# Optimization experiments

Measured on AMD Instinct MI355X. Metric: run time of the kernel, lower is better.

## Reference

```python
import jax, jax.numpy as jnp
import numpy as np

B, S, H, DH, DM = 1024, 32, 32, 32, 1024  # seq==heads==head_dim==32 forced by module's reshapes


def setup_inputs() -> dict:
    key = jax.random.key(0)
    k1, k2 = jax.random.split(key)
    x = jax.random.normal(k1, (B, S, DM), dtype=jnp.float32)
    mask = jnp.ones((1, 1, S, DH), dtype=bool)
    W_qkv = jax.random.normal(k2, (DM, 3 * H * DH), dtype=jnp.float32) / np.sqrt(DM).astype(np.float32)
    return {"x": x, "mask": mask, "W_qkv": W_qkv}


def _rope(t, sin, cos):
    # t: [B, S, H, DH]; sin/cos: [S] broadcast over the HEADS axis (axis 2), as in the original
    t1, t2 = jnp.split(t, 2, axis=-1)
    rot = jnp.concatenate([-t2, t1], axis=-1)
    return t * cos.reshape(1, 1, -1, 1) + rot * sin.reshape(1, 1, -1, 1)


def reference(x, mask, W_qkv):
    b, seq_len, _ = x.shape
    qkv = x @ W_qkv  # [B, S, 3*H*DH]
    q, k, v = jnp.split(qkv, 3, axis=-1)
    q = q.reshape(b, -1, H, DH)
    k = k.reshape(b, -1, H, DH)
    v = v.reshape(b, -1, H, DH)
    pos = jnp.arange(seq_len, dtype=x.dtype)
    sin, cos = jnp.sin(pos), jnp.cos(pos)
    q = _rope(q, sin, cos)
    k = _rope(k, sin, cos)
    # matmul over heads axis (faithful to original): [B,S,H,DH] @ [B,S,DH,H] -> [B,S,H,H]
    attn = jnp.matmul(q, k.transpose(0, 1, 3, 2)) / jnp.sqrt(jnp.asarray(DH, x.dtype))
    attn = attn.reshape(b, H, seq_len, DH)  # valid only because H == 32
    attn = jnp.where(jnp.broadcast_to(mask, attn.shape), attn, -jnp.inf)
    attn = jax.nn.softmax(attn, axis=-1)
    out = jnp.matmul(attn, v)  # [B,H,S,DH] @ [B,S,H,DH]; batched since S==H==32
    return out.reshape(-1, seq_len, H * DH)
```

## Files before the change

### kernel.cpp

```cpp
#include <hip/hip_runtime.h>

typedef __bf16 bf16_t;
typedef __bf16 bf16x4 __attribute__((ext_vector_type(4)));
typedef __bf16 bf16x8 __attribute__((ext_vector_type(8)));
typedef float f32x4 __attribute__((ext_vector_type(4)));
typedef float f32x16 __attribute__((ext_vector_type(16)));
typedef unsigned int uint4v __attribute__((ext_vector_type(4)));

#define M_TOT 32768
#define N_TOT 3072
#define K_TOT 1024

#define WT_BYTES (3072u * 1024u * 2u)
#define XB_BYTES ((size_t)M_TOT * 1024 * 2)

__device__ __forceinline__ void gload_lds16(const void* g, void* l) {
  __builtin_amdgcn_global_load_lds(
      (const __attribute__((address_space(1))) unsigned int*)g,
      (__attribute__((address_space(3))) unsigned int*)l, 16, 0, 0);
}

__device__ __forceinline__ unsigned pk2(float a, float b) {
  unsigned short lo = __builtin_bit_cast(unsigned short, (bf16_t)a);
  unsigned short hi = __builtin_bit_cast(unsigned short, (bf16_t)b);
  return ((unsigned)hi << 16) | (unsigned)lo;
}

__global__ __launch_bounds__(256) void k_wt(const float* __restrict__ W,
                                            bf16_t* __restrict__ wt) {
  __shared__ float tile[64][65];
  const int c0 = blockIdx.x * 64, k0 = blockIdx.y * 64;
  const int t = threadIdx.x;
  for (int rep = 0; rep < 16; ++rep) {
    int lin = rep * 256 + t;
    int kl = lin >> 6, cl = lin & 63;
    tile[kl][cl] = W[(size_t)(k0 + kl) * 3072 + (c0 + cl)];
  }
  __syncthreads();
  const float scale = 0.17677669529663687f;
  for (int rep = 0; rep < 16; ++rep) {
    int lin = rep * 256 + t;
    int cl = lin >> 6, kl = lin & 63;
    int c = c0 + cl;
    float val;
    if (c < 2048) {
      int cc = c & 1023;
      int h = cc >> 5, d = cc & 31;
      float cv = cosf((float)h), sv = sinf((float)h);
      int clp = cl + ((d < 16) ? 16 : -16);
      float other = tile[kl][clp];
      val = tile[kl][cl] * cv + ((d < 16) ? -other : other) * sv;
      if (c < 1024) val *= scale;
    } else {
      val = tile[kl][cl];
    }
    wt[(size_t)c * 1024 + (k0 + kl)] = (bf16_t)val;
  }
}

__global__ __launch_bounds__(256) void k_xb(const float* __restrict__ x,
                                            bf16_t* __restrict__ xb) {
  const size_t nf4 = (size_t)M_TOT * K_TOT / 4;
  const float4* src = (const float4*)x;
  for (size_t i = (size_t)blockIdx.x * 256 + threadIdx.x; i < nf4;
       i += (size_t)gridDim.x * 256) {
    float4 a = src[i];
    bf16x4 o;
    o[0] = (bf16_t)a.x; o[1] = (bf16_t)a.y; o[2] = (bf16_t)a.z; o[3] = (bf16_t)a.w;
    *(bf16x4*)(&xb[i * 4]) = o;
  }
}

__global__ __launch_bounds__(256) void k_gemm(const bf16_t* __restrict__ xb,
                                              const bf16_t* __restrict__ wt,
                                              bf16_t* __restrict__ qk,
                                              bf16_t* __restrict__ vb) {
  __shared__ __attribute__((aligned(16))) bf16_t Al[128 * 32];
  __shared__ __attribute__((aligned(16))) bf16_t Bl[128 * 32];
  const int t = threadIdx.x;
  const int w = t >> 6, lane = t & 63;
  const int wr = w >> 1, wc = w & 1;
  const int row0 = blockIdx.y * 128, col0 = blockIdx.x * 128;

  f32x4 acc[4][4];
  for (int m = 0; m < 4; ++m)
    for (int n = 0; n < 4; ++n)
      for (int i = 0; i < 4; ++i) acc[m][n][i] = 0.f;

  const char* abase = (const char*)xb + (size_t)row0 * 2048;
  const char* bbase = (const char*)wt + (size_t)col0 * 2048;
  const int rsel = lane & 15, ksel = (lane >> 4) * 8;

  for (int kt = 0; kt < 32; ++kt) {
    const int kbyte = kt * 64;
#pragma unroll
    for (int p = 0; p < 2; ++p) {
      const int chunk = w * 2 + p;
      const int o = chunk * 1024 + lane * 16;
      const int trow = o >> 6, twithin = o & 63;
      gload_lds16(abase + (size_t)trow * 2048 + kbyte + twithin, (char*)Al + chunk * 1024);
      gload_lds16(bbase + (size_t)trow * 2048 + kbyte + twithin, (char*)Bl + chunk * 1024);
    }
    __syncthreads();
    bf16x8 a[4], b[4];
#pragma unroll
    for (int m = 0; m < 4; ++m)
      a[m] = *(const bf16x8*)&Al[(wr * 64 + m * 16 + rsel) * 32 + ksel];
#pragma unroll
    for (int n = 0; n < 4; ++n)
      b[n] = *(const bf16x8*)&Bl[(wc * 64 + n * 16 + rsel) * 32 + ksel];
#pragma unroll
    for (int m = 0; m < 4; ++m)
#pragma unroll
      for (int n = 0; n < 4; ++n)
        acc[m][n] = __builtin_amdgcn_mfma_f32_16x16x32_bf16(a[m], b[n], acc[m][n], 0, 0, 0);
    __syncthreads();
  }

  const bool isv = (col0 >= 2048);
  const int rgrp = (lane >> 4) * 4;
#pragma unroll
  for (int m = 0; m < 4; ++m)
#pragma unroll
    for (int n = 0; n < 4; ++n)
#pragma unroll
      for (int reg = 0; reg < 4; ++reg) {
        const int R = row0 + wr * 64 + m * 16 + rgrp + reg;
        const int C = col0 + wc * 64 + n * 16 + rsel;
        const bf16_t val = (bf16_t)acc[m][n][reg];
        if (!isv) qk[(size_t)R * 2048 + C] = val;
        else      vb[(size_t)R * 1024 + (C - 2048)] = val;
      }
}

__global__ __launch_bounds__(256) void k_attn(const bf16_t* __restrict__ qk,
                                              const bf16_t* __restrict__ vb,
                                              float* __restrict__ out) {
  __shared__ __attribute__((aligned(16))) bf16_t vl[4][1024];
  const int t = threadIdx.x;
  const int w = t >> 6, lane = t & 63;
  const int r = blockIdx.x * 4 + w;
  const int jm = lane & 31, hi = lane >> 5;

  const char* vsrc = (const char*)vb + (size_t)r * 2048;
  gload_lds16(vsrc + lane * 16, (char*)vl[w]);
  gload_lds16(vsrc + 1024 + lane * 16, (char*)vl[w] + 1024);

  const char* rowbase = (const char*)qk + (size_t)r * 4096;
  const bf16x8 ak0 = *(const bf16x8*)(rowbase + 2048 + jm * 64 + hi * 16);
  const bf16x8 ak1 = *(const bf16x8*)(rowbase + 2048 + jm * 64 + 32 + hi * 16);
  const bf16x8 bq0 = *(const bf16x8*)(rowbase + jm * 64 + hi * 16);
  const bf16x8 bq1 = *(const bf16x8*)(rowbase + jm * 64 + 32 + hi * 16);

  f32x16 s;
  for (int i = 0; i < 16; ++i) s[i] = 0.f;
  s = __builtin_amdgcn_mfma_f32_32x32x16_bf16(ak0, bq0, s, 0, 0, 0);
  s = __builtin_amdgcn_mfma_f32_32x32x16_bf16(ak1, bq1, s, 0, 0, 0);

  float mx = s[0];
#pragma unroll
  for (int i = 1; i < 16; ++i) mx = fmaxf(mx, s[i]);
  mx = fmaxf(mx, __shfl_xor(mx, 32));
  float p[16];
  float sum = 0.f;
#pragma unroll
  for (int i = 0; i < 16; ++i) { p[i] = __expf(s[i] - mx); sum += p[i]; }
  sum += __shfl_xor(sum, 32);
  const float inv = 1.f / sum;
#pragma unroll
  for (int i = 0; i < 16; ++i) p[i] *= inv;

  const unsigned t01 = pk2(p[0], p[1]),  t23 = pk2(p[2], p[3]);
  const unsigned t45 = pk2(p[4], p[5]),  t67 = pk2(p[6], p[7]);
  const unsigned t89 = pk2(p[8], p[9]),  tab = pk2(p[10], p[11]);
  const unsigned tcd = pk2(p[12], p[13]), tef = pk2(p[14], p[15]);
  const unsigned x01 = (unsigned)__shfl_xor((int)t01, 32), x23 = (unsigned)__shfl_xor((int)t23, 32);
  const unsigned x45 = (unsigned)__shfl_xor((int)t45, 32), x67 = (unsigned)__shfl_xor((int)t67, 32);
  const unsigned x89 = (unsigned)__shfl_xor((int)t89, 32), xab = (unsigned)__shfl_xor((int)tab, 32);
  const unsigned xcd = (unsigned)__shfl_xor((int)tcd, 32), xef = (unsigned)__shfl_xor((int)tef, 32);
  uint4v u0, u1;
  u0[0] = hi ? x45 : t01; u0[1] = hi ? x67 : t23; u0[2] = hi ? t45 : x01; u0[3] = hi ? t67 : x23;
  u1[0] = hi ? xcd : t89; u1[1] = hi ? xef : tab; u1[2] = hi ? tcd : x89; u1[3] = hi ? tef : xab;
  const bf16x8 pa0 = __builtin_bit_cast(bf16x8, u0);
  const bf16x8 pa1 = __builtin_bit_cast(bf16x8, u1);

  asm volatile("s_waitcnt vmcnt(0)" ::: "memory");
  union { bf16x8 v; bf16_t e[8]; } v0, v1;
#pragma unroll
  for (int e = 0; e < 8; ++e) v0.e[e] = vl[w][(8 * hi + e) * 32 + jm];
#pragma unroll
  for (int e = 0; e < 8; ++e) v1.e[e] = vl[w][(16 + 8 * hi + e) * 32 + jm];

  f32x16 o;
  for (int i = 0; i < 16; ++i) o[i] = 0.f;
  o = __builtin_amdgcn_mfma_f32_32x32x16_bf16(pa0, v0.v, o, 0, 0, 0);
  o = __builtin_amdgcn_mfma_f32_32x32x16_bf16(pa1, v1.v, o, 0, 0, 0);

  float* orow = out + (size_t)r * 1024;
#pragma unroll
  for (int reg = 0; reg < 16; ++reg) {
    const int jrow = (reg & 3) + 8 * (reg >> 2) + 4 * hi;
    orow[jrow * 32 + jm] = o[reg];
  }
}

extern "C" void kernel_launch(void* const* d_in, const int* in_sizes, int n_in,
                              void* d_out, int out_size, void* d_ws, size_t ws_size,
                              hipStream_t stream) {
  const float* x = (const float*)d_in[0];
  const float* W = (const float*)d_in[2];

  char* ws = (char*)d_ws;
  bf16_t* wt = (bf16_t*)ws;
  bf16_t* xb = (bf16_t*)(ws + WT_BYTES);
  bf16_t* vb = (bf16_t*)(ws + WT_BYTES + XB_BYTES);

  k_wt <<<dim3(48, 16), 256, 0, stream>>>(W, wt);
  k_xb <<<16384, 256, 0, stream>>>(x, xb);
  k_gemm<<<dim3(24, 256), 256, 0, stream>>>(xb, wt, (bf16_t*)d_out, vb);
  k_attn<<<8192, 256, 0, stream>>>((const bf16_t*)d_out, vb, (float*)d_out);
}
```

Baseline: 338.1 us.

## Rewrite QKV GEMM with triple-buffered LDS pipeline, larger tiles, swizzled layout

Replaces the simple single-buffered GEMM with a 256x128 tile per 512-thread block and a K-step of 64 elements. Tiles flow through a three-slot LDS ring filled by direct global-to-LDS loads, with fine-grained waitcnt/barrier interleaving and raised MFMA priority. It also adds an XOR-swizzled LDS layout against bank conflicts and a block-index swizzle for L2 locality. The aim is to overlap memory loads with MFMA work and cut per-iteration sync overhead, at the cost of much more complex hand-scheduled code and fragile vmcnt accounting.

```diff
diff --git a/kernel.cpp b/kernel.cpp
--- a/kernel.cpp
+++ b/kernel.cpp
@@ -13,6 +13,11 @@
 
 #define WT_BYTES (3072u * 1024u * 2u)
 #define XB_BYTES ((size_t)M_TOT * 1024 * 2)
+
+#define BKB 128
+#define ABYTES 32768
+#define BBYTES 16384
+#define SLOT_BYTES (ABYTES + BBYTES)
 
 __device__ __forceinline__ void gload_lds16(const void* g, void* l) {
   __builtin_amdgcn_global_load_lds(
@@ -71,51 +76,136 @@
   }
 }
 
-__global__ __launch_bounds__(256) void k_gemm(const bf16_t* __restrict__ xb,
-                                              const bf16_t* __restrict__ wt,
-                                              bf16_t* __restrict__ qk,
-                                              bf16_t* __restrict__ vb) {
-  __shared__ __attribute__((aligned(16))) bf16_t Al[128 * 32];
-  __shared__ __attribute__((aligned(16))) bf16_t Bl[128 * 32];
-  const int t = threadIdx.x;
-  const int w = t >> 6, lane = t & 63;
+template <int STAGE, int BW>
+__device__ __forceinline__ void gemm_tile(char* slotR, char* slotW, int tstage,
+                                          const char* const (&asrc)[4],
+                                          const char* const (&bsrc)[2],
+                                          int w, int abase_off, int bbase_off,
+                                          int koff0, f32x4 (&acc)[4][4]) {
+  bf16x8 bfr[4][2];
+  bf16x8 af0[2][2], af1[2][2];
+  const int koff1 = koff0 ^ 64;
+
+  if constexpr (STAGE) {
+    gload_lds16(asrc[0] + (size_t)tstage * BKB, slotW + 0 * 8192 + w * 1024);
+    gload_lds16(asrc[1] + (size_t)tstage * BKB, slotW + 1 * 8192 + w * 1024);
+    gload_lds16(asrc[2] + (size_t)tstage * BKB, slotW + 2 * 8192 + w * 1024);
+  }
+#pragma unroll
+  for (int n = 0; n < 4; ++n) {
+    bfr[n][0] = *(const bf16x8*)(slotR + bbase_off + n * 2048 + koff0);
+    bfr[n][1] = *(const bf16x8*)(slotR + bbase_off + n * 2048 + koff1);
+  }
+#pragma unroll
+  for (int m = 0; m < 2; ++m) {
+    af0[m][0] = *(const bf16x8*)(slotR + abase_off + m * 2048 + koff0);
+    af0[m][1] = *(const bf16x8*)(slotR + abase_off + m * 2048 + koff1);
+  }
+  asm volatile("s_waitcnt lgkmcnt(8)" ::: "memory");
+  __builtin_amdgcn_s_barrier();
+  asm volatile("s_waitcnt lgkmcnt(0)" ::: "memory");
+  __builtin_amdgcn_sched_barrier(0);
+  __builtin_amdgcn_s_setprio(1);
+#pragma unroll
+  for (int m = 0; m < 2; ++m)
+#pragma unroll
+    for (int n = 0; n < 4; ++n) {
+      acc[m][n] = __builtin_amdgcn_mfma_f32_16x16x32_bf16(af0[m][0], bfr[n][0], acc[m][n], 0, 0, 0);
+      acc[m][n] = __builtin_amdgcn_mfma_f32_16x16x32_bf16(af0[m][1], bfr[n][1], acc[m][n], 0, 0, 0);
+    }
+  __builtin_amdgcn_s_setprio(0);
+  __builtin_amdgcn_s_barrier();
+
+  if constexpr (STAGE) {
+    gload_lds16(asrc[3] + (size_t)tstage * BKB, slotW + 3 * 8192 + w * 1024);
+    gload_lds16(bsrc[0] + (size_t)tstage * BKB, slotW + ABYTES + 0 * 8192 + w * 1024);
+    gload_lds16(bsrc[1] + (size_t)tstage * BKB, slotW + ABYTES + 1 * 8192 + w * 1024);
+  }
+#pragma unroll
+  for (int m = 0; m < 2; ++m) {
+    af1[m][0] = *(const bf16x8*)(slotR + abase_off + (m + 2) * 2048 + koff0);
+    af1[m][1] = *(const bf16x8*)(slotR + abase_off + (m + 2) * 2048 + koff1);
+  }
+  __builtin_amdgcn_s_barrier();
+  asm volatile("s_waitcnt lgkmcnt(0)" ::: "memory");
+  __builtin_amdgcn_sched_barrier(0);
+  __builtin_amdgcn_s_setprio(1);
+#pragma unroll
+  for (int m = 0; m < 2; ++m)
+#pragma unroll
+    for (int n = 0; n < 4; ++n) {
+      acc[m + 2][n] = __builtin_amdgcn_mfma_f32_16x16x32_bf16(af1[m][0], bfr[n][0], acc[m + 2][n], 0, 0, 0);
+      acc[m + 2][n] = __builtin_amdgcn_mfma_f32_16x16x32_bf16(af1[m][1], bfr[n][1], acc[m + 2][n], 0, 0, 0);
+    }
+  __builtin_amdgcn_s_setprio(0);
+  if constexpr (BW == 6) asm volatile("s_waitcnt vmcnt(6)" ::: "memory");
+  else if constexpr (BW == 0) asm volatile("s_waitcnt vmcnt(0)" ::: "memory");
+  __builtin_amdgcn_s_barrier();
+}
+
+__global__ __launch_bounds__(512, 2) void k_gemm(const bf16_t* __restrict__ xb,
+                                                 const bf16_t* __restrict__ wt,
+                                                 bf16_t* __restrict__ qk,
+                                                 bf16_t* __restrict__ vb) {
+  __shared__ __attribute__((aligned(16))) char lds[3 * SLOT_BYTES];
+  const int tid = threadIdx.x;
+  const int w = tid >> 6, lane = tid & 63;
   const int wr = w >> 1, wc = w & 1;
-  const int row0 = blockIdx.y * 128, col0 = blockIdx.x * 128;
+
+  const int bid = blockIdx.x;
+  const int swz = (bid & 7) * 384 + (bid >> 3);
+  const int tm = swz / 24, tn = swz % 24;
+  const int row0 = tm * 256, col0 = tn * 128;
+
+  const int l8 = lane >> 3, l7 = lane & 7;
+  const int awithin = (l7 * 16) ^ (l8 << 4);
+  const char* asrc[4];
+  const char* bsrc[2];
+#pragma unroll
+  for (int i = 0; i < 4; ++i)
+    asrc[i] = (const char*)xb + (size_t)(row0 + i * 64 + w * 8 + l8) * 2048 + awithin;
+#pragma unroll
+  for (int i = 0; i < 2; ++i)
+    bsrc[i] = (const char*)wt + (size_t)(col0 + i * 64 + w * 8 + l8) * 2048 + awithin;
+
+  const int rsel = lane & 15;
+  const int koff0 = ((lane >> 4) * 16) ^ (l7 << 4);
+  const int abase_off = (wr * 64 + rsel) * 128;
+  const int bbase_off = ABYTES + (wc * 64 + rsel) * 128;
 
   f32x4 acc[4][4];
+#pragma unroll
   for (int m = 0; m < 4; ++m)
+#pragma unroll
     for (int n = 0; n < 4; ++n)
+#pragma unroll
       for (int i = 0; i < 4; ++i) acc[m][n][i] = 0.f;
 
-  const char* abase = (const char*)xb + (size_t)row0 * 2048;
-  const char* bbase = (const char*)wt + (size_t)col0 * 2048;
-  const int rsel = lane & 15, ksel = (lane >> 4) * 8;
-
-  for (int kt = 0; kt < 32; ++kt) {
-    const int kbyte = kt * 64;
-#pragma unroll
-    for (int p = 0; p < 2; ++p) {
-      const int chunk = w * 2 + p;
-      const int o = chunk * 1024 + lane * 16;
-      const int trow = o >> 6, twithin = o & 63;
-      gload_lds16(abase + (size_t)trow * 2048 + kbyte + twithin, (char*)Al + chunk * 1024);
-      gload_lds16(bbase + (size_t)trow * 2048 + kbyte + twithin, (char*)Bl + chunk * 1024);
-    }
-    __syncthreads();
-    bf16x8 a[4], b[4];
-#pragma unroll
-    for (int m = 0; m < 4; ++m)
-      a[m] = *(const bf16x8*)&Al[(wr * 64 + m * 16 + rsel) * 32 + ksel];
-#pragma unroll
-    for (int n = 0; n < 4; ++n)
-      b[n] = *(const bf16x8*)&Bl[(wc * 64 + n * 16 + rsel) * 32 + ksel];
-#pragma unroll
-    for (int m = 0; m < 4; ++m)
-#pragma unroll
-      for (int n = 0; n < 4; ++n)
-        acc[m][n] = __builtin_amdgcn_mfma_f32_16x16x32_bf16(a[m], b[n], acc[m][n], 0, 0, 0);
-    __syncthreads();
-  }
+  {
+    char* s0 = lds;
+    char* s1 = lds + SLOT_BYTES;
+#pragma unroll
+    for (int i = 0; i < 4; ++i) gload_lds16(asrc[i], s0 + i * 8192 + w * 1024);
+#pragma unroll
+    for (int i = 0; i < 2; ++i) gload_lds16(bsrc[i], s0 + ABYTES + i * 8192 + w * 1024);
+#pragma unroll
+    for (int i = 0; i < 4; ++i) gload_lds16(asrc[i] + BKB, s1 + i * 8192 + w * 1024);
+#pragma unroll
+    for (int i = 0; i < 2; ++i) gload_lds16(bsrc[i] + BKB, s1 + ABYTES + i * 8192 + w * 1024);
+    asm volatile("s_waitcnt vmcnt(6)" ::: "memory");
+    __builtin_amdgcn_s_barrier();
+  }
+
+  int sr = 0;
+  for (int t = 0; t < 14; ++t) {
+    char* slotR = lds + sr * SLOT_BYTES;
+    const int swi = (sr >= 1) ? sr - 1 : 2;
+    char* slotW = lds + swi * SLOT_BYTES;
+    gemm_tile<1, 6>(slotR, slotW, t + 2, asrc, bsrc, w, abase_off, bbase_off, koff0, acc);
+    sr = (sr == 2) ? 0 : sr + 1;
+  }
+  gemm_tile<0, 0>(lds + 2 * SLOT_BYTES, lds, 0, asrc, bsrc, w, abase_off, bbase_off, koff0, acc);
+  gemm_tile<0, -1>(lds, lds, 0, asrc, bsrc, w, abase_off, bbase_off, koff0, acc);
 
   const bool isv = (col0 >= 2048);
   const int rgrp = (lane >> 4) * 4;
@@ -217,6 +307,6 @@
 
   k_wt <<<dim3(48, 16), 256, 0, stream>>>(W, wt);
   k_xb <<<16384, 256, 0, stream>>>(x, xb);
-  k_gemm<<<dim3(24, 256), 256, 0, stream>>>(xb, wt, (bf16_t*)d_out, vb);
+  k_gemm<<<3072, 512, 0, stream>>>(xb, wt, (bf16_t*)d_out, vb);
   k_attn<<<8192, 256, 0, stream>>>((const bf16_t*)d_out, vb, (float*)d_out);
 }
```

New measurement: 334.7 us. No clear change (-1.0%).

## Rewrite QKV GEMM with 256x256 tiles, double-buffered LDS and swizzled pipeline

Applied to the files above, without the earlier changes.

The QKV projection GEMM moves from 128x128 tiles with a synchronous single-buffer loop to 256x256 tiles on 512 threads, with a 64-wide K step. LDS is double-buffered, and global-to-LDS loads for the next tile are interleaved with MFMA phases under fine-grained barriers and s_setprio. It also adds an XOR swizzle on LDS addresses to avoid bank conflicts and a block-index swizzle for L2 locality. The aim is to hide memory latency and raise MFMA utilisation. In exchange, register pressure rises (128 accumulator floats per thread) and the hand-placed waitcnt/barrier ordering becomes fragile.

```diff
diff --git a/kernel.cpp b/kernel.cpp
--- a/kernel.cpp
+++ b/kernel.cpp
@@ -13,6 +13,9 @@
 
 #define WT_BYTES (3072u * 1024u * 2u)
 #define XB_BYTES ((size_t)M_TOT * 1024 * 2)
+
+#define BREG 32768
+#define SLOT 65536
 
 __device__ __forceinline__ void gload_lds16(const void* g, void* l) {
   __builtin_amdgcn_global_load_lds(
@@ -71,62 +74,178 @@
   }
 }
 
-__global__ __launch_bounds__(256) void k_gemm(const bf16_t* __restrict__ xb,
-                                              const bf16_t* __restrict__ wt,
-                                              bf16_t* __restrict__ qk,
-                                              bf16_t* __restrict__ vb) {
-  __shared__ __attribute__((aligned(16))) bf16_t Al[128 * 32];
-  __shared__ __attribute__((aligned(16))) bf16_t Bl[128 * 32];
-  const int t = threadIdx.x;
-  const int w = t >> 6, lane = t & 63;
-  const int wr = w >> 1, wc = w & 1;
-  const int row0 = blockIdx.y * 128, col0 = blockIdx.x * 128;
-
-  f32x4 acc[4][4];
+template <int FINAL>
+__device__ __forceinline__ void ktile(const char* sR, char* sW,
+                                      const char* aT, const char* bT, int w,
+                                      int aoff0, int boff0,
+                                      f32x4 (&acc)[8][4]) {
+  bf16x8 a[4][2], b[4][2];
+
+  if constexpr (!FINAL) {
+    gload_lds16(aT, sW + w * 1024);
+    gload_lds16(aT + 64 * 2048, sW + 8192 + w * 1024);
+  }
+#pragma unroll
+  for (int m = 0; m < 4; ++m) {
+    const int o = aoff0 + m * 4096;
+    a[m][0] = *(const bf16x8*)(sR + o);
+    a[m][1] = *(const bf16x8*)(sR + (o ^ 64));
+  }
+#pragma unroll
+  for (int n = 0; n < 2; ++n) {
+    const int o = boff0 + n * 8192;
+    b[n][0] = *(const bf16x8*)(sR + o);
+    b[n][1] = *(const bf16x8*)(sR + (o ^ 64));
+  }
+  asm volatile("s_waitcnt lgkmcnt(8)" ::: "memory");
+  __builtin_amdgcn_s_barrier();
+  asm volatile("s_waitcnt lgkmcnt(0)" ::: "memory");
+  __builtin_amdgcn_sched_barrier(0);
+  __builtin_amdgcn_s_setprio(1);
+#pragma unroll
   for (int m = 0; m < 4; ++m)
+#pragma unroll
+    for (int n = 0; n < 2; ++n) {
+      acc[m][n] = __builtin_amdgcn_mfma_f32_16x16x32_bf16(a[m][0], b[n][0], acc[m][n], 0, 0, 0);
+      acc[m][n] = __builtin_amdgcn_mfma_f32_16x16x32_bf16(a[m][1], b[n][1], acc[m][n], 0, 0, 0);
+    }
+  __builtin_amdgcn_s_setprio(0);
+  if constexpr (!FINAL) asm volatile("s_waitcnt vmcnt(4)" ::: "memory");
+  else                  asm volatile("s_waitcnt vmcnt(2)" ::: "memory");
+  __builtin_amdgcn_s_barrier();
+
+  if constexpr (!FINAL) {
+    gload_lds16(bT, sW + BREG + w * 1024);
+    gload_lds16(bT + 64 * 2048, sW + BREG + 8192 + w * 1024);
+  }
+#pragma unroll
+  for (int n = 2; n < 4; ++n) {
+    const int o = boff0 + n * 8192;
+    b[n][0] = *(const bf16x8*)(sR + o);
+    b[n][1] = *(const bf16x8*)(sR + (o ^ 64));
+  }
+  __builtin_amdgcn_s_barrier();
+  asm volatile("s_waitcnt lgkmcnt(0)" ::: "memory");
+  __builtin_amdgcn_sched_barrier(0);
+  __builtin_amdgcn_s_setprio(1);
+#pragma unroll
+  for (int m = 0; m < 4; ++m)
+#pragma unroll
+    for (int n = 2; n < 4; ++n) {
+      acc[m][n] = __builtin_amdgcn_mfma_f32_16x16x32_bf16(a[m][0], b[n][0], acc[m][n], 0, 0, 0);
+      acc[m][n] = __builtin_amdgcn_mfma_f32_16x16x32_bf16(a[m][1], b[n][1], acc[m][n], 0, 0, 0);
+    }
+  __builtin_amdgcn_s_setprio(0);
+  if constexpr (!FINAL) asm volatile("s_waitcnt vmcnt(4)" ::: "memory");
+  else                  asm volatile("s_waitcnt vmcnt(0)" ::: "memory");
+  __builtin_amdgcn_s_barrier();
+
+  if constexpr (!FINAL) {
+    gload_lds16(bT + 128 * 2048, sW + BREG + 16384 + w * 1024);
+    gload_lds16(bT + 192 * 2048, sW + BREG + 24576 + w * 1024);
+  }
+#pragma unroll
+  for (int m = 0; m < 4; ++m) {
+    const int o = aoff0 + (m + 4) * 4096;
+    a[m][0] = *(const bf16x8*)(sR + o);
+    a[m][1] = *(const bf16x8*)(sR + (o ^ 64));
+  }
+  __builtin_amdgcn_s_barrier();
+  asm volatile("s_waitcnt lgkmcnt(0)" ::: "memory");
+  __builtin_amdgcn_sched_barrier(0);
+  __builtin_amdgcn_s_setprio(1);
+#pragma unroll
+  for (int m = 0; m < 4; ++m)
+#pragma unroll
+    for (int n = 2; n < 4; ++n) {
+      acc[m + 4][n] = __builtin_amdgcn_mfma_f32_16x16x32_bf16(a[m][0], b[n][0], acc[m + 4][n], 0, 0, 0);
+      acc[m + 4][n] = __builtin_amdgcn_mfma_f32_16x16x32_bf16(a[m][1], b[n][1], acc[m + 4][n], 0, 0, 0);
+    }
+  __builtin_amdgcn_s_setprio(0);
+  __builtin_amdgcn_s_barrier();
+
+  if constexpr (!FINAL) {
+    gload_lds16(aT + 128 * 2048, sW + 16384 + w * 1024);
+    gload_lds16(aT + 192 * 2048, sW + 24576 + w * 1024);
+  }
+  __builtin_amdgcn_s_barrier();
+  __builtin_amdgcn_s_setprio(1);
+#pragma unroll
+  for (int m = 0; m < 4; ++m)
+#pragma unroll
+    for (int n = 0; n < 2; ++n) {
+      acc[m + 4][n] = __builtin_amdgcn_mfma_f32_16x16x32_bf16(a[m][0], b[n][0], acc[m + 4][n], 0, 0, 0);
+      acc[m + 4][n] = __builtin_amdgcn_mfma_f32_16x16x32_bf16(a[m][1], b[n][1], acc[m + 4][n], 0, 0, 0);
+    }
+  __builtin_amdgcn_s_setprio(0);
+  if constexpr (!FINAL) asm volatile("s_waitcnt vmcnt(4)" ::: "memory");
+  __builtin_amdgcn_s_barrier();
+}
+
+__global__ __launch_bounds__(512, 2) void k_gemm(const bf16_t* __restrict__ xb,
+                                                 const bf16_t* __restrict__ wt,
+                                                 bf16_t* __restrict__ qk,
+                                                 bf16_t* __restrict__ vb) {
+  __shared__ __attribute__((aligned(16))) char lds[2 * SLOT];
+  const int tid = threadIdx.x;
+  const int w = tid >> 6, lane = tid & 63;
+  const int wr = w >> 2, wc = w & 3;
+
+  const int bid = blockIdx.x;
+  const int swz = (bid & 7) * 192 + (bid >> 3);
+  const int tm = swz / 12, tn = swz % 12;
+  const int row0 = tm * 256, col0 = tn * 256;
+
+  const int l8 = lane >> 3, l7 = lane & 7;
+  const int awithin = (l7 * 16) ^ (l8 << 4);
+  const char* aT0 = (const char*)xb + (size_t)(row0 + w * 8 + l8) * 2048 + awithin;
+  const char* bT0 = (const char*)wt + (size_t)(col0 + w * 8 + l8) * 2048 + awithin;
+
+  const int rsel = lane & 15;
+  const int koff0 = ((lane >> 4) * 16) ^ (l7 << 4);
+  const int aoff0 = (wr * 16 + rsel) * 128 + koff0;
+  const int boff0 = BREG + (wc * 16 + rsel) * 128 + koff0;
+
+  f32x4 acc[8][4];
+#pragma unroll
+  for (int m = 0; m < 8; ++m)
+#pragma unroll
     for (int n = 0; n < 4; ++n)
+#pragma unroll
       for (int i = 0; i < 4; ++i) acc[m][n][i] = 0.f;
 
-  const char* abase = (const char*)xb + (size_t)row0 * 2048;
-  const char* bbase = (const char*)wt + (size_t)col0 * 2048;
-  const int rsel = lane & 15, ksel = (lane >> 4) * 8;
-
-  for (int kt = 0; kt < 32; ++kt) {
-    const int kbyte = kt * 64;
-#pragma unroll
-    for (int p = 0; p < 2; ++p) {
-      const int chunk = w * 2 + p;
-      const int o = chunk * 1024 + lane * 16;
-      const int trow = o >> 6, twithin = o & 63;
-      gload_lds16(abase + (size_t)trow * 2048 + kbyte + twithin, (char*)Al + chunk * 1024);
-      gload_lds16(bbase + (size_t)trow * 2048 + kbyte + twithin, (char*)Bl + chunk * 1024);
-    }
-    __syncthreads();
-    bf16x8 a[4], b[4];
-#pragma unroll
-    for (int m = 0; m < 4; ++m)
-      a[m] = *(const bf16x8*)&Al[(wr * 64 + m * 16 + rsel) * 32 + ksel];
-#pragma unroll
-    for (int n = 0; n < 4; ++n)
-      b[n] = *(const bf16x8*)&Bl[(wc * 64 + n * 16 + rsel) * 32 + ksel];
-#pragma unroll
-    for (int m = 0; m < 4; ++m)
-#pragma unroll
-      for (int n = 0; n < 4; ++n)
-        acc[m][n] = __builtin_amdgcn_mfma_f32_16x16x32_bf16(a[m], b[n], acc[m][n], 0, 0, 0);
-    __syncthreads();
-  }
+  {
+    char* s0 = lds;
+    gload_lds16(aT0, s0 + w * 1024);
+    gload_lds16(aT0 + 64 * 2048, s0 + 8192 + w * 1024);
+    gload_lds16(bT0, s0 + BREG + w * 1024);
+    gload_lds16(bT0 + 64 * 2048, s0 + BREG + 8192 + w * 1024);
+    gload_lds16(bT0 + 128 * 2048, s0 + BREG + 16384 + w * 1024);
+    gload_lds16(bT0 + 192 * 2048, s0 + BREG + 24576 + w * 1024);
+    gload_lds16(aT0 + 128 * 2048, s0 + 16384 + w * 1024);
+    gload_lds16(aT0 + 192 * 2048, s0 + 24576 + w * 1024);
+    asm volatile("s_waitcnt vmcnt(4)" ::: "memory");
+    __builtin_amdgcn_s_barrier();
+  }
+
+  for (int t = 0; t < 15; ++t) {
+    const char* sR = lds + (t & 1) * SLOT;
+    char* sW = lds + ((t + 1) & 1) * SLOT;
+    ktile<0>(sR, sW, aT0 + (size_t)(t + 1) * 128, bT0 + (size_t)(t + 1) * 128,
+             w, aoff0, boff0, acc);
+  }
+  ktile<1>(lds + SLOT, lds, aT0, bT0, w, aoff0, boff0, acc);
 
   const bool isv = (col0 >= 2048);
   const int rgrp = (lane >> 4) * 4;
 #pragma unroll
-  for (int m = 0; m < 4; ++m)
+  for (int m = 0; m < 8; ++m)
 #pragma unroll
     for (int n = 0; n < 4; ++n)
 #pragma unroll
       for (int reg = 0; reg < 4; ++reg) {
-        const int R = row0 + wr * 64 + m * 16 + rgrp + reg;
-        const int C = col0 + wc * 64 + n * 16 + rsel;
+        const int R = row0 + wr * 16 + m * 32 + rgrp + reg;
+        const int C = col0 + wc * 16 + n * 64 + rsel;
         const bf16_t val = (bf16_t)acc[m][n][reg];
         if (!isv) qk[(size_t)R * 2048 + C] = val;
         else      vb[(size_t)R * 1024 + (C - 2048)] = val;
@@ -217,6 +336,6 @@
 
   k_wt <<<dim3(48, 16), 256, 0, stream>>>(W, wt);
   k_xb <<<16384, 256, 0, stream>>>(x, xb);
-  k_gemm<<<dim3(24, 256), 256, 0, stream>>>(xb, wt, (bf16_t*)d_out, vb);
+  k_gemm<<<1536, 512, 0, stream>>>(xb, wt, (bf16_t*)d_out, vb);
   k_attn<<<8192, 256, 0, stream>>>((const bf16_t*)d_out, vb, (float*)d_out);
 }
```

New measurement: 292.6 us. 13.4% less time.

## Rewrite QKV GEMM with 256x256 tiles, triple-buffered LDS pipeline and swizzling

Applied to the files above, without the earlier changes.

Replaces the 128x128 single-buffered GEMM with a 512-thread 256x256-tile kernel. It uses a three-slot LDS ring fed by global_load_lds, an XOR-swizzled LDS layout, interleaved MFMA and LDS reads with setprio and sched barriers, and a block-index swizzle for L2 locality. The goal is to hide global-load latency, cut the per-iteration barrier count and raise data reuse per tile. It adds heavy register pressure from 32 accumulator tiles and fragile hand-written waitcnt sequencing.

```diff
diff --git a/kernel.cpp b/kernel.cpp
--- a/kernel.cpp
+++ b/kernel.cpp
@@ -13,6 +13,8 @@
 
 #define WT_BYTES (3072u * 1024u * 2u)
 #define XB_BYTES ((size_t)M_TOT * 1024 * 2)
+
+#define SLOT 32768
 
 __device__ __forceinline__ void gload_lds16(const void* g, void* l) {
   __builtin_amdgcn_global_load_lds(
@@ -71,62 +73,153 @@
   }
 }
 
-__global__ __launch_bounds__(256) void k_gemm(const bf16_t* __restrict__ xb,
-                                              const bf16_t* __restrict__ wt,
-                                              bf16_t* __restrict__ qk,
-                                              bf16_t* __restrict__ vb) {
-  __shared__ __attribute__((aligned(16))) bf16_t Al[128 * 32];
-  __shared__ __attribute__((aligned(16))) bf16_t Bl[128 * 32];
-  const int t = threadIdx.x;
-  const int w = t >> 6, lane = t & 63;
-  const int wr = w >> 1, wc = w & 1;
-  const int row0 = blockIdx.y * 128, col0 = blockIdx.x * 128;
-
-  f32x4 acc[4][4];
-  for (int m = 0; m < 4; ++m)
+template <int MODE>
+__device__ __forceinline__ void ktile(const char* sR, const char* sRn, char* sW,
+                                      const char* aT, const char* bT, int w,
+                                      int aoffLo, int boffLo,
+                                      f32x4 (&acc)[8][4],
+                                      bf16x8 (&a)[4], bf16x8 (&b)[4]) {
+  bf16x8 a2[4];
+
+  if constexpr (MODE == 0) gload_lds16(aT, sW + w * 1024);
+  b[2] = *(const bf16x8*)(sR + (boffLo ^ 64));
+  b[3] = *(const bf16x8*)(sR + ((boffLo + 8192) ^ 64));
+  asm volatile("s_waitcnt lgkmcnt(2)" ::: "memory");
+  __builtin_amdgcn_sched_barrier(0);
+  __builtin_amdgcn_s_setprio(1);
+#pragma unroll
+  for (int m = 0; m < 4; ++m)
+#pragma unroll
+    for (int n = 0; n < 2; ++n)
+      acc[m][n] = __builtin_amdgcn_mfma_f32_16x16x32_bf16(a[m], b[n], acc[m][n], 0, 0, 0);
+  __builtin_amdgcn_s_setprio(0);
+
+  if constexpr (MODE == 0) gload_lds16(bT, sW + 16384 + w * 1024);
+#pragma unroll
+  for (int m = 0; m < 4; ++m)
+    a2[m] = *(const bf16x8*)(sR + ((aoffLo + m * 4096) ^ 64));
+  asm volatile("s_waitcnt lgkmcnt(4)" ::: "memory");
+  __builtin_amdgcn_sched_barrier(0);
+  __builtin_amdgcn_s_setprio(1);
+#pragma unroll
+  for (int m = 0; m < 4; ++m)
+#pragma unroll
+    for (int n = 2; n < 4; ++n)
+      acc[m][n] = __builtin_amdgcn_mfma_f32_16x16x32_bf16(a[m], b[n], acc[m][n], 0, 0, 0);
+  __builtin_amdgcn_s_setprio(0);
+
+  if constexpr (MODE == 0) gload_lds16(aT + 64 * 2048, sW + 8192 + w * 1024);
+  asm volatile("s_waitcnt lgkmcnt(0)" ::: "memory");
+  __builtin_amdgcn_sched_barrier(0);
+  __builtin_amdgcn_s_setprio(1);
+#pragma unroll
+  for (int m = 0; m < 4; ++m)
+#pragma unroll
+    for (int n = 2; n < 4; ++n)
+      acc[m + 4][n] = __builtin_amdgcn_mfma_f32_16x16x32_bf16(a2[m], b[n], acc[m + 4][n], 0, 0, 0);
+  __builtin_amdgcn_s_setprio(0);
+
+  if constexpr (MODE == 0) {
+    gload_lds16(bT + 64 * 2048, sW + 24576 + w * 1024);
+    asm volatile("s_waitcnt vmcnt(4)" ::: "memory");
+  } else if constexpr (MODE == 1) {
+    asm volatile("s_waitcnt vmcnt(0)" ::: "memory");
+  }
+  if constexpr (MODE <= 1) {
+    __builtin_amdgcn_s_barrier();
+    __builtin_amdgcn_sched_barrier(0);
+#pragma unroll
+    for (int m = 0; m < 4; ++m)
+      a[m] = *(const bf16x8*)(sRn + aoffLo + m * 4096);
+    __builtin_amdgcn_sched_barrier(0);
+  }
+  __builtin_amdgcn_s_setprio(1);
+#pragma unroll
+  for (int m = 0; m < 4; ++m)
+#pragma unroll
+    for (int n = 0; n < 2; ++n)
+      acc[m + 4][n] = __builtin_amdgcn_mfma_f32_16x16x32_bf16(a2[m], b[n], acc[m + 4][n], 0, 0, 0);
+  __builtin_amdgcn_s_setprio(0);
+  if constexpr (MODE <= 1) {
+    b[0] = *(const bf16x8*)(sRn + boffLo);
+    b[1] = *(const bf16x8*)(sRn + boffLo + 8192);
+  }
+}
+
+__global__ __launch_bounds__(512, 2) void k_gemm(const bf16_t* __restrict__ xb,
+                                                 const bf16_t* __restrict__ wt,
+                                                 bf16_t* __restrict__ qk,
+                                                 bf16_t* __restrict__ vb) {
+  __shared__ __attribute__((aligned(16))) char lds[3 * SLOT];
+  const int tid = threadIdx.x;
+  const int w = tid >> 6, lane = tid & 63;
+  const int wr = w >> 2, wc = w & 3;
+
+  const int bid = blockIdx.x;
+  const int swz = (bid & 7) * 192 + (bid >> 3);
+  const int tm = swz / 12, tn = swz % 12;
+  const int row0 = tm * 256, col0 = tn * 256;
+
+  const int j = lane >> 3;
+  const int u = (lane & 7) ^ j;
+  const int half = u >> 2, kk = u & 3;
+  const char* aS = (const char*)xb + (size_t)(row0 + half * 128 + w * 8 + j) * 2048 + kk * 16;
+  const char* bS = (const char*)wt + (size_t)(col0 + half * 128 + w * 8 + j) * 2048 + kk * 16;
+
+  const int rsel = lane & 15, kslot = lane >> 4;
+  const int kswz = ((kslot ^ (rsel & 7)) << 4);
+  const int aoffLo = (wr * 16 + rsel) * 128 + kswz;
+  const int boffLo = 16384 + (wc * 16 + rsel) * 128 + kswz;
+
+  f32x4 acc[8][4];
+#pragma unroll
+  for (int m = 0; m < 8; ++m)
+#pragma unroll
     for (int n = 0; n < 4; ++n)
+#pragma unroll
       for (int i = 0; i < 4; ++i) acc[m][n][i] = 0.f;
 
-  const char* abase = (const char*)xb + (size_t)row0 * 2048;
-  const char* bbase = (const char*)wt + (size_t)col0 * 2048;
-  const int rsel = lane & 15, ksel = (lane >> 4) * 8;
-
-  for (int kt = 0; kt < 32; ++kt) {
-    const int kbyte = kt * 64;
-#pragma unroll
-    for (int p = 0; p < 2; ++p) {
-      const int chunk = w * 2 + p;
-      const int o = chunk * 1024 + lane * 16;
-      const int trow = o >> 6, twithin = o & 63;
-      gload_lds16(abase + (size_t)trow * 2048 + kbyte + twithin, (char*)Al + chunk * 1024);
-      gload_lds16(bbase + (size_t)trow * 2048 + kbyte + twithin, (char*)Bl + chunk * 1024);
-    }
-    __syncthreads();
-    bf16x8 a[4], b[4];
+  bf16x8 a[4], b[4];
+
+  {
+    gload_lds16(aS,                lds + w * 1024);
+    gload_lds16(bS,                lds + 16384 + w * 1024);
+    gload_lds16(aS + 64 * 2048,    lds + 8192 + w * 1024);
+    gload_lds16(bS + 64 * 2048,    lds + 24576 + w * 1024);
+    gload_lds16(aS + 64,             lds + SLOT + w * 1024);
+    gload_lds16(bS + 64,             lds + SLOT + 16384 + w * 1024);
+    gload_lds16(aS + 64 * 2048 + 64, lds + SLOT + 8192 + w * 1024);
+    gload_lds16(bS + 64 * 2048 + 64, lds + SLOT + 24576 + w * 1024);
+    asm volatile("s_waitcnt vmcnt(4)" ::: "memory");
+    __builtin_amdgcn_s_barrier();
+    __builtin_amdgcn_sched_barrier(0);
 #pragma unroll
     for (int m = 0; m < 4; ++m)
-      a[m] = *(const bf16x8*)&Al[(wr * 64 + m * 16 + rsel) * 32 + ksel];
-#pragma unroll
-    for (int n = 0; n < 4; ++n)
-      b[n] = *(const bf16x8*)&Bl[(wc * 64 + n * 16 + rsel) * 32 + ksel];
-#pragma unroll
-    for (int m = 0; m < 4; ++m)
-#pragma unroll
-      for (int n = 0; n < 4; ++n)
-        acc[m][n] = __builtin_amdgcn_mfma_f32_16x16x32_bf16(a[m], b[n], acc[m][n], 0, 0, 0);
-    __syncthreads();
-  }
+      a[m] = *(const bf16x8*)(lds + aoffLo + m * 4096);
+    b[0] = *(const bf16x8*)(lds + boffLo);
+    b[1] = *(const bf16x8*)(lds + boffLo + 8192);
+  }
+
+  int s0 = 0, s1 = 1, s2 = 2;
+  for (int t = 0; t < 30; ++t) {
+    ktile<0>(lds + s0 * SLOT, lds + s1 * SLOT, lds + s2 * SLOT,
+             aS + (size_t)(t + 2) * 64, bS + (size_t)(t + 2) * 64,
+             w, aoffLo, boffLo, acc, a, b);
+    const int tmp = s0; s0 = s1; s1 = s2; s2 = tmp;
+  }
+  ktile<1>(lds + s0 * SLOT, lds + s1 * SLOT, lds, aS, bS, w, aoffLo, boffLo, acc, a, b);
+  ktile<2>(lds + s1 * SLOT, lds, lds, aS, bS, w, aoffLo, boffLo, acc, a, b);
 
   const bool isv = (col0 >= 2048);
   const int rgrp = (lane >> 4) * 4;
 #pragma unroll
-  for (int m = 0; m < 4; ++m)
+  for (int m = 0; m < 8; ++m)
 #pragma unroll
     for (int n = 0; n < 4; ++n)
 #pragma unroll
       for (int reg = 0; reg < 4; ++reg) {
-        const int R = row0 + wr * 64 + m * 16 + rgrp + reg;
-        const int C = col0 + wc * 64 + n * 16 + rsel;
+        const int R = row0 + wr * 16 + m * 32 + rgrp + reg;
+        const int C = col0 + wc * 16 + n * 64 + rsel;
         const bf16_t val = (bf16_t)acc[m][n][reg];
         if (!isv) qk[(size_t)R * 2048 + C] = val;
         else      vb[(size_t)R * 1024 + (C - 2048)] = val;
@@ -217,6 +310,6 @@
 
   k_wt <<<dim3(48, 16), 256, 0, stream>>>(W, wt);
   k_xb <<<16384, 256, 0, stream>>>(x, xb);
-  k_gemm<<<dim3(24, 256), 256, 0, stream>>>(xb, wt, (bf16_t*)d_out, vb);
+  k_gemm<<<1536, 512, 0, stream>>>(xb, wt, (bf16_t*)d_out, vb);
   k_attn<<<8192, 256, 0, stream>>>((const bf16_t*)d_out, vb, (float*)d_out);
 }
```

Result: faster. 301.5 us (-10.8%).
